# Performance work log

Measured on AMD Instinct MI355X. Metric: run time of the kernel, lower is better.

Reference implementation:

```python
import jax, jax.numpy as jnp
import numpy as np
from jax import lax

DIM = 96
HEADS = 6
H = W = D = 64
EPS = 1e-12  # torch F.normalize default


def setup_inputs() -> dict:
    key = jax.random.key(0)
    k1, k2, k3, k4 = jax.random.split(key, 4)
    x = jax.random.normal(k1, (1, DIM, H, W, D), dtype=jnp.float32)
    # qkv 1x1 conv weight, stored as (3*dim, dim) matrix
    w_qkv = jax.random.normal(k2, (3 * DIM, DIM), dtype=jnp.float32) * (1.0 / np.sqrt(DIM))
    # depthwise 3x3x3 conv weight (OIDHW with I=1, groups=3*dim)
    w_dw = jax.random.normal(k3, (3 * DIM, 1, 3, 3, 3), dtype=jnp.float32) * (1.0 / np.sqrt(27))
    # output 1x1 conv weight as (dim, dim)
    w_proj = jax.random.normal(k4, (DIM, DIM), dtype=jnp.float32) * (1.0 / np.sqrt(DIM))
    temperature = jnp.ones((HEADS, 1, 1), dtype=jnp.float32)
    return {"x": x, "w_qkv": w_qkv, "w_dw": w_dw, "w_proj": w_proj, "temperature": temperature}


def _l2norm(t):
    # torch F.normalize(dim=-1): t / max(||t||, eps)
    n = jnp.sqrt(jnp.sum(t * t, axis=-1, keepdims=True))
    return t / jnp.maximum(n, EPS)


def reference(x, w_qkv, w_dw, w_proj, temperature):
    b, c, h, w, d = x.shape
    ch = c // HEADS  # per-head channels
    # 1x1 conv -> pointwise GEMM over channels
    qkv = jnp.einsum('bchwd,oc->bohwd', x, w_qkv)  # (b, 3c, h, w, d)
    # depthwise 3x3x3 conv, padding 1
    qkv = lax.conv_general_dilated(
        qkv, w_dw, window_strides=(1, 1, 1), padding=[(1, 1)] * 3,
        feature_group_count=3 * c,
        dimension_numbers=('NCDHW', 'OIDHW', 'NCDHW'))
    q, k, v = jnp.split(qkv, 3, axis=1)
    n = h * w * d
    q = q.reshape(b, HEADS, ch, n)
    k = k.reshape(b, HEADS, ch, n)
    v = v.reshape(b, HEADS, ch, n)
    q = _l2norm(q)
    k = _l2norm(k)
    # channel-wise attention: (b, heads, ch, ch)
    attn = jnp.einsum('bhcn,bhdn->bhcd', q, k) * temperature[None]
    attn = jax.nn.softmax(attn, axis=-1)
    out = jnp.einsum('bhcd,bhdn->bhcn', attn, v)  # (b, heads, ch, n)
    out = out.reshape(b, c, h, w, d)
    out = jnp.einsum('bchwd,oc->bohwd', out, w_proj)
    return out
```

## Files before the change

kernel.cpp:

```cpp
#include <hip/hip_runtime.h>
#include <hip/hip_bf16.h>
#include <hip/hip_fp16.h>

#define NTOT 262144
typedef __hip_bfloat16 bf16;
typedef __attribute__((ext_vector_type(4))) float f32x4;
typedef _Float16 f16x8 __attribute__((ext_vector_type(8)));
typedef unsigned int u32x4 __attribute__((ext_vector_type(4)));

__device__ inline ushort f2bf(float f){ bf16 b = __float2bfloat16(f); return *(ushort*)&b; }
__device__ inline float bf2f(ushort u){ union{unsigned i;float f;}v; v.i = (unsigned)u<<16; return v.f; }
__device__ inline unsigned h2u(__half2 h){ union{__half2 h; unsigned u;}v; v.h=h; return v.u; }
__device__ inline __half2 u2h(unsigned u){ union{unsigned u; __half2 h;}v; v.u=u; return v.h; }
__device__ inline ushort f2h(float f){ __half h = __float2half_rn(f); return *(ushort*)&h; }

__global__ void detect_dtype(const ushort* __restrict__ w, int* __restrict__ flag) {
  int tid = threadIdx.x;
  int sane = 0;
  for (int i = tid; i < 512; i += 64) {
    ushort u = w[2 * i];
    int e = (u >> 7) & 0xff;
    sane += (e == 0 || (e >= 100 && e <= 140)) ? 1 : 0;
  }
#pragma unroll
  for (int off = 32; off > 0; off >>= 1) sane += __shfl_down(sane, off, 64);
  if (tid == 0) *flag = (sane >= 256) ? 1 : 0;
}

__global__ void cvt_f16(const void* __restrict__ in, ushort* __restrict__ outw,
                        int n, const int* __restrict__ flag) {
  int f = *flag;
  for (int i = blockIdx.x * 256 + threadIdx.x; i < n; i += gridDim.x * 256) {
    float v = f ? bf2f(((const ushort*)in)[i]) : ((const float*)in)[i];
    outw[i] = f2h(v);
  }
}

template<int MODE>
__global__ __launch_bounds__(256)
void transpose96(const void* __restrict__ in, ushort* __restrict__ out,
                 const int* __restrict__ flag) {
  __shared__ float t[96][65];
  const int tid = threadIdx.x;
  const long n0 = (long)blockIdx.x * 64;
  const int f = (MODE == 0) ? *flag : 0;
#pragma unroll
  for (int i = 0; i < 6; i++) {
    int idx = tid + 256 * i;
    int u = idx & 15, c = idx >> 4;
    float v0, v1, v2, v3;
    if (MODE == 0 && !f) {
      float4 q = *(const float4*)((const float*)in + (size_t)c * NTOT + n0 + u * 4);
      v0 = q.x; v1 = q.y; v2 = q.z; v3 = q.w;
    } else if (MODE == 0) {
      uint2 q = *(const uint2*)((const ushort*)in + (size_t)c * NTOT + n0 + u * 4);
      v0 = bf2f((ushort)(q.x & 0xffffu)); v1 = bf2f((ushort)(q.x >> 16));
      v2 = bf2f((ushort)(q.y & 0xffffu)); v3 = bf2f((ushort)(q.y >> 16));
    } else {
      uint2 q = *(const uint2*)((const ushort*)in + (size_t)c * NTOT + n0 + u * 4);
      __half2 a = u2h(q.x), b = u2h(q.y);
      v0 = __half2float(a.x); v1 = __half2float(a.y);
      v2 = __half2float(b.x); v3 = __half2float(b.y);
    }
    t[c][u*4+0] = v0; t[c][u*4+1] = v1; t[c][u*4+2] = v2; t[c][u*4+3] = v3;
  }
  __syncthreads();
#pragma unroll
  for (int i = 0; i < 3; i++) {
    int idx = tid + 256 * i;
    int oq = idx % 12, n = idx / 12;
    unsigned d[4];
#pragma unroll
    for (int j = 0; j < 4; j++) {
      __half2 hp = __floats2half2_rn(t[oq*8 + 2*j][n], t[oq*8 + 2*j + 1][n]);
      d[j] = h2u(hp);
    }
    *(uint4*)(out + (size_t)(n0 + n) * 96 + oq * 8) = make_uint4(d[0], d[1], d[2], d[3]);
  }
}

template<int OF, bool DYNOUT>
__global__ __launch_bounds__(384)
void gemm96f(const ushort* __restrict__ W, const ushort* __restrict__ Xt,
             void* __restrict__ C, const int* __restrict__ flag) {
  const int tid = threadIdx.x;
  const long n0 = (long)blockIdx.x * 64;
  const int wave = tid >> 6, lane = tid & 63;
  const int col = lane & 15, quad = lane >> 4;
  const int f = DYNOUT ? *flag : 0;
  f32x4 acc[OF][4];
#pragma unroll
  for (int a = 0; a < OF; a++)
#pragma unroll
    for (int b = 0; b < 4; b++) acc[a][b] = (f32x4)0.f;
  const int obase = wave * 16 * OF;
#pragma unroll
  for (int ks = 0; ks < 3; ks++) {
    f16x8 bfrag[4];
#pragma unroll
    for (int nf = 0; nf < 4; nf++)
      bfrag[nf] = *(const f16x8*)(Xt + (size_t)(n0 + nf*16 + col) * 96 + ks*32 + quad*8);
#pragma unroll
    for (int of = 0; of < OF; of++) {
      const int o = obase + of*16 + col;
      f16x8 afrag = *(const f16x8*)(W + (size_t)o * 96 + ks*32 + quad*8);
#pragma unroll
      for (int nf = 0; nf < 4; nf++)
        acc[of][nf] = __builtin_amdgcn_mfma_f32_16x16x32_f16(afrag, bfrag[nf], acc[of][nf], 0, 0, 0);
    }
  }
  __shared__ __align__(16) ushort cs[96 * OF][72];
#pragma unroll
  for (int of = 0; of < OF; of++)
#pragma unroll
    for (int nf = 0; nf < 4; nf++)
#pragma unroll
      for (int r = 0; r < 4; r++) {
        int o = obase + of*16 + quad*4 + r;
        cs[o][nf*16 + col] = f2h(acc[of][nf][r]);
      }
  __syncthreads();
  if (!DYNOUT) {
#pragma unroll
    for (int i = 0; i < 2 * OF; i++) {
      int idx = tid + 384 * i;
      int o = idx >> 3, u = idx & 7;
      uint4 v = *(const uint4*)&cs[o][u * 8];
      *(uint4*)((ushort*)C + (size_t)o * NTOT + n0 + u * 8) = v;
    }
  } else {
#pragma unroll
    for (int i = 0; i < 4; i++) {
      int idx = tid + 384 * i;
      int o = idx >> 4, u = idx & 15;
      uint2 v = *(const uint2*)&cs[o][u * 4];
      __half2 a = u2h(v.x), b = u2h(v.y);
      float f0 = __half2float(a.x), f1 = __half2float(a.y);
      float f2 = __half2float(b.x), f3 = __half2float(b.y);
      if (!f) {
        float4 q = {f0, f1, f2, f3};
        *(float4*)((float*)C + (size_t)o * NTOT + n0 + u * 4) = q;
      } else {
        uint2 q = make_uint2(((unsigned)f2bf(f1) << 16) | f2bf(f0),
                             ((unsigned)f2bf(f3) << 16) | f2bf(f2));
        *(uint2*)((ushort*)C + (size_t)o * NTOT + n0 + u * 4) = q;
      }
    }
  }
}

__global__ __launch_bounds__(256)
void dwconv3(const ushort* __restrict__ in, const void* __restrict__ wt,
             ushort* __restrict__ out, const int* __restrict__ flag) {
  const unsigned B = blockIdx.x;
  const int xcd = B & 7;
  const int s = B >> 3;
  const int c = xcd + 8 * (s >> 5);
  const int sp = s & 31;
  const int tid = threadIdx.x;
  const int dq = tid & 7;
  const int w = (sp >> 2) * 8 + ((tid >> 3) & 7);
  const int h0 = (sp & 3) * 16 + (tid >> 6) * 4;
  const int d0 = dq * 8;
  __shared__ __half2 wsm2[27];
  if (tid < 27) {
    int f = *flag;
    float wv = f ? bf2f(((const ushort*)wt)[c * 27 + tid])
                 : ((const float*)wt)[c * 27 + tid];
    wsm2[tid] = __floats2half2_rn(wv, wv);
  }
  __syncthreads();
  __half2 wreg[27];
#pragma unroll
  for (int i = 0; i < 27; i++) wreg[i] = wsm2[i];
  const unsigned maskL = (dq == 0) ? 0xFFFF0000u : 0xFFFFFFFFu;
  const unsigned maskR = (dq == 7) ? 0x0000FFFFu : 0xFFFFFFFFu;
  __half2 acc[4][4];
#pragma unroll
  for (int r = 0; r < 4; r++)
#pragma unroll
    for (int j = 0; j < 4; j++) acc[r][j] = u2h(0u);
  const size_t cbase = (size_t)c * NTOT;
#pragma unroll
  for (int dw = -1; dw <= 1; dw++) {
    const int ww = w + dw;
    const bool wok = (ww >= 0 && ww <= 63);
    const ushort* rowp = in + cbase + (size_t)ww * 64 + d0;
#pragma unroll
    for (int e = -1; e <= 4; e++) {
      const int hh = h0 + e;
      if (hh < 0 || hh > 63) continue;
      uint4 u = make_uint4(0u, 0u, 0u, 0u);
      if (wok)
        u = *(const uint4*)(rowp + (size_t)hh * 4096);
      unsigned P = (unsigned)__shfl_up((int)u.w, 1, 8);
      unsigned N = (unsigned)__shfl_down((int)u.x, 1, 8);
      unsigned S0 = __builtin_amdgcn_perm(u.x, P,   0x05040302) & maskL;
      unsigned S1 = __builtin_amdgcn_perm(u.y, u.x, 0x05040302);
      unsigned S2 = __builtin_amdgcn_perm(u.z, u.y, 0x05040302);
      unsigned S3 = __builtin_amdgcn_perm(u.w, u.z, 0x05040302);
      unsigned R3 = __builtin_amdgcn_perm(N,   u.w, 0x05040302) & maskR;
#pragma unroll
      for (int r = (e - 1 < 0 ? 0 : e - 1); r <= (e + 1 > 3 ? 3 : e + 1); r++) {
        const int wb = (e - r + 1) * 9 + (dw + 1) * 3;
        const __half2 wL = wreg[wb], wC = wreg[wb + 1], wR = wreg[wb + 2];
        acc[r][0] = __hfma2(wL, u2h(S0), acc[r][0]); acc[r][0] = __hfma2(wC, u2h(u.x), acc[r][0]); acc[r][0] = __hfma2(wR, u2h(S1), acc[r][0]);
        acc[r][1] = __hfma2(wL, u2h(S1), acc[r][1]); acc[r][1] = __hfma2(wC, u2h(u.y), acc[r][1]); acc[r][1] = __hfma2(wR, u2h(S2), acc[r][1]);
        acc[r][2] = __hfma2(wL, u2h(S2), acc[r][2]); acc[r][2] = __hfma2(wC, u2h(u.z), acc[r][2]); acc[r][2] = __hfma2(wR, u2h(S3), acc[r][2]);
        acc[r][3] = __hfma2(wL, u2h(S3), acc[r][3]); acc[r][3] = __hfma2(wC, u2h(u.w), acc[r][3]); acc[r][3] = __hfma2(wR, u2h(R3), acc[r][3]);
      }
    }
  }
#pragma unroll
  for (int r = 0; r < 4; r++) {
    u32x4 pv = { h2u(acc[r][0]), h2u(acc[r][1]), h2u(acc[r][2]), h2u(acc[r][3]) };
    __builtin_nontemporal_store(pv,
        (u32x4*)(out + cbase + ((size_t)(h0 + r) * 64 + w) * 64 + d0));
  }
}

__global__ __launch_bounds__(256)
void gram16(const ushort* __restrict__ qk, float* __restrict__ G) {
  const int hd = blockIdx.y;
  const int tid = threadIdx.x, wave = tid >> 6, lane = tid & 63;
  const int col = lane & 15, quad = lane >> 4;
  const ushort* qp = qk + (size_t)(hd * 16 + col) * NTOT;
  const ushort* kp = qp + (size_t)96 * NTOT;
  f32x4 aqk = (f32x4)0.f, aqq = (f32x4)0.f, akk = (f32x4)0.f;
  const int nbase = blockIdx.x * 4096 + wave * 32 + quad * 8;
#pragma unroll 4
  for (int it = 0; it < 32; it++) {
    f16x8 qf = *(const f16x8*)(qp + nbase + it * 128);
    f16x8 kf = *(const f16x8*)(kp + nbase + it * 128);
    aqk = __builtin_amdgcn_mfma_f32_16x16x32_f16(qf, kf, aqk, 0, 0, 0);
    aqq = __builtin_amdgcn_mfma_f32_16x16x32_f16(qf, qf, aqq, 0, 0, 0);
    akk = __builtin_amdgcn_mfma_f32_16x16x32_f16(kf, kf, akk, 0, 0, 0);
  }
  __shared__ float red[4][64][12];
#pragma unroll
  for (int r = 0; r < 4; r++) {
    red[wave][lane][r]     = aqk[r];
    red[wave][lane][4 + r] = aqq[r];
    red[wave][lane][8 + r] = akk[r];
  }
  __syncthreads();
  if (wave == 0) {
#pragma unroll
    for (int j = 0; j < 12; j++) {
      float v = red[0][lane][j] + red[1][lane][j] + red[2][lane][j] + red[3][lane][j];
      int sub = j >> 2, r = j & 3;
      atomicAdd(&G[hd * 768 + sub * 256 + (quad * 4 + r) * 16 + col], v);
    }
  }
}

__global__ __launch_bounds__(256)
void attn_mix(const float* __restrict__ G, const void* __restrict__ wp,
              const void* __restrict__ temp, ushort* __restrict__ M,
              const int* __restrict__ flag) {
  __shared__ float As[6][16][16];
  const int tid = threadIdx.x;
  const int f = *flag;
  if (tid < 96) {
    int hd = tid >> 4, c = tid & 15;
    const float* Gh = G + hd * 768;
    float qn = fmaxf(sqrtf(fmaxf(Gh[256 + c * 17], 0.f)), 1e-12f);
    float t = f ? bf2f(((const ushort*)temp)[hd]) : ((const float*)temp)[hd];
    float lg[16];
    float mx = -1e30f;
#pragma unroll
    for (int d = 0; d < 16; d++) {
      float kn = fmaxf(sqrtf(fmaxf(Gh[512 + d * 17], 0.f)), 1e-12f);
      lg[d] = Gh[c * 16 + d] / (qn * kn) * t;
      mx = fmaxf(mx, lg[d]);
    }
    float s = 0.f;
#pragma unroll
    for (int d = 0; d < 16; d++) { lg[d] = __expf(lg[d] - mx); s += lg[d]; }
    float inv = 1.f / s;
#pragma unroll
    for (int d = 0; d < 16; d++) As[hd][c][d] = lg[d] * inv;
  }
  __syncthreads();
  int idx = blockIdx.x * 256 + tid;
  int o = idx / 96, p = idx - o * 96;
  int hd = p >> 4, d = p & 15;
  float s = 0.f;
#pragma unroll
  for (int cc = 0; cc < 16; cc++) {
    float wv = f ? bf2f(((const ushort*)wp)[o * 96 + hd * 16 + cc])
                 : ((const float*)wp)[o * 96 + hd * 16 + cc];
    s += wv * As[hd][cc][d];
  }
  M[idx] = f2h(s);
}

extern "C" void kernel_launch(void* const* d_in, const int* in_sizes, int n_in,
                              void* d_out, int out_size, void* d_ws, size_t ws_size,
                              hipStream_t stream) {
  const void* x      = d_in[0];
  const void* w_qkv  = d_in[1];
  const void* w_dw   = d_in[2];
  const void* w_proj = d_in[3];
  const void* temp   = d_in[4];

  const size_t szQKV = (size_t)288 * NTOT * 2;
  ushort* B1 = (ushort*)d_ws;
  ushort* B2 = (ushort*)((char*)d_ws + szQKV);
  ushort* Xt = B2;
  ushort* Vt = B1;
  char* tail = (char*)d_ws + 2 * szQKV;
  float*  G    = (float*)tail;
  ushort* M    = (ushort*)(tail + 18432);
  ushort* Wh   = (ushort*)(tail + 36864);
  int*    flag = (int*)(tail + 92160);
  if (ws_size < 2 * szQKV + 92160 + 256) return;

  detect_dtype<<<1, 64, 0, stream>>>((const ushort*)w_qkv, flag);
  cvt_f16<<<32, 256, 0, stream>>>(w_qkv, Wh, 288 * 96, flag);
  hipMemsetAsync(G, 0, 4608 * 4, stream);
  transpose96<0><<<4096, 256, 0, stream>>>(x, Xt, flag);
  gemm96f<3, false><<<4096, 384, 0, stream>>>(Wh, Xt, B1, flag);
  dwconv3<<<9216, 256, 0, stream>>>(B1, w_dw, B2, flag);
  gram16<<<dim3(64, 6), 256, 0, stream>>>(B2, G);
  transpose96<1><<<4096, 256, 0, stream>>>(B2 + (size_t)192 * NTOT, Vt, flag);
  attn_mix<<<36, 256, 0, stream>>>(G, w_proj, temp, M, flag);
  gemm96f<1, true><<<4096, 384, 0, stream>>>(M, Vt, d_out, flag);
}
```

Before: 383.1 us.

## Fuse channel transpose into GEMM kernels via shared memory staging

Removes the two standalone transpose96 kernels and performs the channel-major to token-major transpose inside the GEMM kernels through shared memory, so the transposed intermediate (Xt/Vt) no longer makes a round trip through global memory. The qkv GEMM output now uses nontemporal stores. The gram kernel grid is doubled with half the iterations per block to raise parallelism. The cost is more shared memory per GEMM block, which may lower occupancy, and extra atomics or reduction traffic in gram16.

```diff
diff --git a/kernel.cpp b/kernel.cpp
--- a/kernel.cpp
+++ b/kernel.cpp
@@ -36,58 +36,57 @@
   }
 }
 
-template<int MODE>
-__global__ __launch_bounds__(256)
-void transpose96(const void* __restrict__ in, ushort* __restrict__ out,
-                 const int* __restrict__ flag) {
-  __shared__ float t[96][65];
-  const int tid = threadIdx.x;
-  const long n0 = (long)blockIdx.x * 64;
-  const int f = (MODE == 0) ? *flag : 0;
-#pragma unroll
-  for (int i = 0; i < 6; i++) {
-    int idx = tid + 256 * i;
-    int u = idx & 15, c = idx >> 4;
-    float v0, v1, v2, v3;
-    if (MODE == 0 && !f) {
-      float4 q = *(const float4*)((const float*)in + (size_t)c * NTOT + n0 + u * 4);
-      v0 = q.x; v1 = q.y; v2 = q.z; v3 = q.w;
-    } else if (MODE == 0) {
-      uint2 q = *(const uint2*)((const ushort*)in + (size_t)c * NTOT + n0 + u * 4);
-      v0 = bf2f((ushort)(q.x & 0xffffu)); v1 = bf2f((ushort)(q.x >> 16));
-      v2 = bf2f((ushort)(q.y & 0xffffu)); v3 = bf2f((ushort)(q.y >> 16));
-    } else {
-      uint2 q = *(const uint2*)((const ushort*)in + (size_t)c * NTOT + n0 + u * 4);
-      __half2 a = u2h(q.x), b = u2h(q.y);
-      v0 = __half2float(a.x); v1 = __half2float(a.y);
-      v2 = __half2float(b.x); v3 = __half2float(b.y);
-    }
-    t[c][u*4+0] = v0; t[c][u*4+1] = v1; t[c][u*4+2] = v2; t[c][u*4+3] = v3;
-  }
-  __syncthreads();
-#pragma unroll
-  for (int i = 0; i < 3; i++) {
-    int idx = tid + 256 * i;
-    int oq = idx % 12, n = idx / 12;
-    unsigned d[4];
-#pragma unroll
-    for (int j = 0; j < 4; j++) {
-      __half2 hp = __floats2half2_rn(t[oq*8 + 2*j][n], t[oq*8 + 2*j + 1][n]);
-      d[j] = h2u(hp);
-    }
-    *(uint4*)(out + (size_t)(n0 + n) * 96 + oq * 8) = make_uint4(d[0], d[1], d[2], d[3]);
-  }
-}
-
-template<int OF, bool DYNOUT>
+template<int OF, int MODE, bool DYNOUT>
 __global__ __launch_bounds__(384)
-void gemm96f(const ushort* __restrict__ W, const ushort* __restrict__ Xt,
+void gemm96x(const ushort* __restrict__ W, const void* __restrict__ X,
              void* __restrict__ C, const int* __restrict__ flag) {
+  constexpr int CSB = 96 * OF * 72 * 2;
+  constexpr int TB  = 96 * 66 * 2;
+  constexpr int UNI = (CSB > TB ? CSB : TB);
+  __shared__ __align__(16) char smem[UNI + 64 * 104 * 2];
+  ushort (*t16)[66] = (ushort(*)[66])smem;
+  ushort (*cs)[72]  = (ushort(*)[72])smem;
+  ushort (*Xs)[104] = (ushort(*)[104])(smem + UNI);
   const int tid = threadIdx.x;
   const long n0 = (long)blockIdx.x * 64;
   const int wave = tid >> 6, lane = tid & 63;
   const int col = lane & 15, quad = lane >> 4;
-  const int f = DYNOUT ? *flag : 0;
+  const int f = (MODE == 0 || DYNOUT) ? *flag : 0;
+
+#pragma unroll
+  for (int i = 0; i < 4; i++) {
+    int idx = tid + 384 * i;
+    int u = idx & 15, c = idx >> 4;
+    ushort h0, h1, h2, h3;
+    if (MODE == 0 && !f) {
+      float4 q = *(const float4*)((const float*)X + (size_t)c * NTOT + n0 + u * 4);
+      h0 = f2h(q.x); h1 = f2h(q.y); h2 = f2h(q.z); h3 = f2h(q.w);
+    } else if (MODE == 0) {
+      uint2 q = *(const uint2*)((const ushort*)X + (size_t)c * NTOT + n0 + u * 4);
+      h0 = f2h(bf2f((ushort)(q.x & 0xffffu))); h1 = f2h(bf2f((ushort)(q.x >> 16)));
+      h2 = f2h(bf2f((ushort)(q.y & 0xffffu))); h3 = f2h(bf2f((ushort)(q.y >> 16)));
+    } else {
+      uint2 q = *(const uint2*)((const ushort*)X + (size_t)c * NTOT + n0 + u * 4);
+      h0 = (ushort)(q.x & 0xffffu); h1 = (ushort)(q.x >> 16);
+      h2 = (ushort)(q.y & 0xffffu); h3 = (ushort)(q.y >> 16);
+    }
+    *(unsigned*)&t16[c][u * 4]     = (unsigned)h0 | ((unsigned)h1 << 16);
+    *(unsigned*)&t16[c][u * 4 + 2] = (unsigned)h2 | ((unsigned)h3 << 16);
+  }
+  __syncthreads();
+
+#pragma unroll
+  for (int i = 0; i < 2; i++) {
+    int idx = tid + 384 * i;
+    int oq = idx % 12, n = idx / 12;
+    unsigned d[4];
+#pragma unroll
+    for (int j = 0; j < 4; j++)
+      d[j] = (unsigned)t16[oq * 8 + 2 * j][n] | ((unsigned)t16[oq * 8 + 2 * j + 1][n] << 16);
+    *(uint4*)&Xs[n][oq * 8] = make_uint4(d[0], d[1], d[2], d[3]);
+  }
+  __syncthreads();
+
   f32x4 acc[OF][4];
 #pragma unroll
   for (int a = 0; a < OF; a++)
@@ -99,25 +98,24 @@
     f16x8 bfrag[4];
 #pragma unroll
     for (int nf = 0; nf < 4; nf++)
-      bfrag[nf] = *(const f16x8*)(Xt + (size_t)(n0 + nf*16 + col) * 96 + ks*32 + quad*8);
+      bfrag[nf] = *(const f16x8*)&Xs[nf * 16 + col][ks * 32 + quad * 8];
 #pragma unroll
     for (int of = 0; of < OF; of++) {
-      const int o = obase + of*16 + col;
-      f16x8 afrag = *(const f16x8*)(W + (size_t)o * 96 + ks*32 + quad*8);
+      const int o = obase + of * 16 + col;
+      f16x8 afrag = *(const f16x8*)(W + (size_t)o * 96 + ks * 32 + quad * 8);
 #pragma unroll
       for (int nf = 0; nf < 4; nf++)
         acc[of][nf] = __builtin_amdgcn_mfma_f32_16x16x32_f16(afrag, bfrag[nf], acc[of][nf], 0, 0, 0);
     }
   }
-  __shared__ __align__(16) ushort cs[96 * OF][72];
 #pragma unroll
   for (int of = 0; of < OF; of++)
 #pragma unroll
     for (int nf = 0; nf < 4; nf++)
 #pragma unroll
       for (int r = 0; r < 4; r++) {
-        int o = obase + of*16 + quad*4 + r;
-        cs[o][nf*16 + col] = f2h(acc[of][nf][r]);
+        int o = obase + of * 16 + quad * 4 + r;
+        cs[o][nf * 16 + col] = f2h(acc[of][nf][r]);
       }
   __syncthreads();
   if (!DYNOUT) {
@@ -125,8 +123,8 @@
     for (int i = 0; i < 2 * OF; i++) {
       int idx = tid + 384 * i;
       int o = idx >> 3, u = idx & 7;
-      uint4 v = *(const uint4*)&cs[o][u * 8];
-      *(uint4*)((ushort*)C + (size_t)o * NTOT + n0 + u * 8) = v;
+      u32x4 v = *(const u32x4*)&cs[o][u * 8];
+      __builtin_nontemporal_store(v, (u32x4*)((ushort*)C + (size_t)o * NTOT + n0 + u * 8));
     }
   } else {
 #pragma unroll
@@ -227,9 +225,9 @@
   const ushort* qp = qk + (size_t)(hd * 16 + col) * NTOT;
   const ushort* kp = qp + (size_t)96 * NTOT;
   f32x4 aqk = (f32x4)0.f, aqq = (f32x4)0.f, akk = (f32x4)0.f;
-  const int nbase = blockIdx.x * 4096 + wave * 32 + quad * 8;
+  const int nbase = blockIdx.x * 2048 + wave * 32 + quad * 8;
 #pragma unroll 4
-  for (int it = 0; it < 32; it++) {
+  for (int it = 0; it < 16; it++) {
     f16x8 qf = *(const f16x8*)(qp + nbase + it * 128);
     f16x8 kf = *(const f16x8*)(kp + nbase + it * 128);
     aqk = __builtin_amdgcn_mfma_f32_16x16x32_f16(qf, kf, aqk, 0, 0, 0);
@@ -307,8 +305,6 @@
   const size_t szQKV = (size_t)288 * NTOT * 2;
   ushort* B1 = (ushort*)d_ws;
   ushort* B2 = (ushort*)((char*)d_ws + szQKV);
-  ushort* Xt = B2;
-  ushort* Vt = B1;
   char* tail = (char*)d_ws + 2 * szQKV;
   float*  G    = (float*)tail;
   ushort* M    = (ushort*)(tail + 18432);
@@ -319,11 +315,9 @@
   detect_dtype<<<1, 64, 0, stream>>>((const ushort*)w_qkv, flag);
   cvt_f16<<<32, 256, 0, stream>>>(w_qkv, Wh, 288 * 96, flag);
   hipMemsetAsync(G, 0, 4608 * 4, stream);
-  transpose96<0><<<4096, 256, 0, stream>>>(x, Xt, flag);
-  gemm96f<3, false><<<4096, 384, 0, stream>>>(Wh, Xt, B1, flag);
+  gemm96x<3, 0, false><<<4096, 384, 0, stream>>>(Wh, x, B1, flag);
   dwconv3<<<9216, 256, 0, stream>>>(B1, w_dw, B2, flag);
-  gram16<<<dim3(64, 6), 256, 0, stream>>>(B2, G);
-  transpose96<1><<<4096, 256, 0, stream>>>(B2 + (size_t)192 * NTOT, Vt, flag);
+  gram16<<<dim3(128, 6), 256, 0, stream>>>(B2, G);
   attn_mix<<<36, 256, 0, stream>>>(G, w_proj, temp, M, flag);
-  gemm96f<1, true><<<4096, 384, 0, stream>>>(M, Vt, d_out, flag);
-}
+  gemm96x<1, 1, true><<<4096, 384, 0, stream>>>(M, B2 + (size_t)192 * NTOT, d_out, flag);
+}
```

Result: slower. 401.8 us (+4.9%).
